# Kernel tuning notes

Hardware: AMD Instinct MI355X
Metric: run time of the kernel (lower is better)

## Reference

```python
import jax, jax.numpy as jnp
import numpy as np
from jax import lax

B, T = 16, 1000
IN_DIM = 257
CTX = 3            # left + 1 + right
FEAT = CTX * IN_DIM  # 771
H = 512
L = 2              # SRU layers
KN = 9             # conv kernels
KS = 6             # conv kernel size


def setup_inputs() -> dict:
    key = jax.random.key(0)
    ks = jax.random.split(key, 10)
    n = jax.random.normal
    return {
        "inputs": n(ks[0], (B, T, FEAT), jnp.float32),
        "W_in": n(ks[1], (FEAT, H), jnp.float32) / np.sqrt(FEAT),
        "b_in": jnp.zeros((H,), jnp.float32),
        "W_rnn": n(ks[2], (L, H, 3 * H), jnp.float32) / np.sqrt(H),
        "v_rnn": n(ks[3], (L, 2 * H), jnp.float32) * 0.1,
        "b_rnn": jnp.zeros((L, 2 * H), jnp.float32),
        "conv_k": n(ks[4], (KN, 1, KS, KS), jnp.float32) * 0.05,
        "conv_b": jnp.zeros((KN,), jnp.float32),
        "W_out": n(ks[5], (H * KN, FEAT), jnp.float32) / np.sqrt(H * KN),
        "b_out": jnp.zeros((FEAT,), jnp.float32),
    }


def _sru_layer(x, W, v, b):
    # x: (T, B, H) time-major; SRU: c_t = f_t*c_{t-1} + (1-f_t)*(W x_t),
    # highway h_t = r_t*c_t + (1-r_t)*x_t; gates peek at c_{t-1} via v.
    U = jnp.einsum("tbh,hk->tbk", x, W)          # (T, B, 3H)
    xt, fp, rp = jnp.split(U, 3, axis=-1)
    vf, vr = jnp.split(v, 2)
    bf, br = jnp.split(b, 2)

    def step(c, inp):
        xt_t, fp_t, rp_t, xin_t = inp
        f = jax.nn.sigmoid(fp_t + vf * c + bf)
        c_new = f * c + (1.0 - f) * xt_t
        r = jax.nn.sigmoid(rp_t + vr * c + br)
        h = r * c_new + (1.0 - r) * xin_t
        return c_new, h

    c0 = jnp.zeros(x.shape[1:], x.dtype)
    _, hs = lax.scan(step, c0, (xt, fp, rp, x))
    return hs


def reference(inputs, W_in, b_in, W_rnn, v_rnn, b_rnn, conv_k, conv_b, W_out, b_out):
    # input layer: Linear + Tanh
    h = jnp.tanh(jnp.einsum("btf,fh->bth", inputs, W_in) + b_in)  # (B,T,H)
    x = jnp.transpose(h, (1, 0, 2))                               # (T,B,H)
    for l in range(L):
        x = _sru_layer(x, W_rnn[l], v_rnn[l], b_rnn[l])
    h = jnp.transpose(x, (1, 0, 2))[:, None]                      # (B,1,T,H)

    # Conv2d with asymmetric pad (left/top 3, right/bottom 2), +bias, tanh
    y = lax.conv_general_dilated(
        h, conv_k, window_strides=(1, 1), padding=[(3, 2), (3, 2)],
        dimension_numbers=("NCHW", "OIHW", "NCHW"))
    y = jnp.tanh(y + conv_b[None, :, None, None])                 # (B,KN,T,H)
    # MaxPool2d(3, stride=1, padding=1)
    y = lax.reduce_window(y, -jnp.inf, lax.max, (1, 1, 3, 3), (1, 1, 1, 1),
                          [(0, 0), (0, 0), (1, 1), (1, 1)])

    # (B,KN,T,H) -> (B,T,H,KN) -> (B,T,H*KN)  (matches torch double transpose)
    y = jnp.transpose(y, (0, 2, 3, 1)).reshape(B, T, H * KN)
    mask = jax.nn.sigmoid(jnp.einsum("btf,fo->bto", y, W_out) + b_out)
    out = mask * inputs
    return out[:, :, IN_DIM:2 * IN_DIM]  # center frame (left_context slice)
```

## Files before the change

kernel.cpp:

```cpp
#include <hip/hip_runtime.h>
#include <hip/hip_bf16.h>

#define B_    16
#define T_    1000
#define FEAT  771
#define FEATP 800
#define H_    512
#define H3    1536
#define KN_   9
#define KHID  4608
#define M_    16000
#define NOUT  257
#define KSLICES 3

typedef _Float16 half8 __attribute__((ext_vector_type(8)));
typedef _Float16 half4 __attribute__((ext_vector_type(4)));
typedef _Float16 half2v __attribute__((ext_vector_type(2)));
typedef float    floatx4 __attribute__((ext_vector_type(4)));

__device__ inline float tanh_fast(float z) {
    return 1.0f - 2.0f / (1.0f + __expf(2.0f * z));
}
__device__ inline float sigmoid_fast(float z) {
    return 1.0f / (1.0f + __expf(-z));
}

__device__ inline void gload16(const _Float16* g, _Float16* l) {
    __builtin_amdgcn_global_load_lds(
        (const __attribute__((address_space(1))) void*)g,
        (__attribute__((address_space(3))) void*)l, 16, 0, 0);
}

__global__ void convert_inputs(const float* __restrict__ in, _Float16* __restrict__ A1) {
    size_t i = (size_t)blockIdx.x * 256 + threadIdx.x;
    if (i >= (size_t)M_ * FEATP) return;
    size_t r = i / FEATP;
    int   cc = (int)(i % FEATP);
    A1[i] = (cc < FEAT) ? (_Float16)in[r * FEAT + cc] : (_Float16)0.f;
}

__global__ __launch_bounds__(256) void transpose_w(
    const float* __restrict__ W, _Float16* __restrict__ Wt,
    int K, int N, int ldw, int coloff, int Kp, int perm9)
{
    __shared__ float tile[32][33];
    const int kb = blockIdx.x * 32;
    const int nb = blockIdx.y * 32;
    const int tx = threadIdx.x & 31;
    const int ty = threadIdx.x >> 5;
    #pragma unroll
    for (int r = ty; r < 32; r += 8) {
        const int k = kb + r, n = nb + tx;
        tile[r][tx] = (k < K && n < N) ? W[(size_t)k * ldw + coloff + n] : 0.f;
    }
    __syncthreads();
    #pragma unroll
    for (int r = ty; r < 32; r += 8) {
        const int n = nb + r, k = kb + tx;
        if (n < N && k < Kp) {
            size_t kidx = (size_t)k;
            if (perm9) kidx = (size_t)(k % 9) * 512 + (size_t)(k / 9);
            Wt[(size_t)n * Kp + kidx] = (_Float16)tile[tx][r];
        }
    }
}

template <int EPI>
__global__ __launch_bounds__(256) void gemm_kernel(
    const _Float16* __restrict__ A, const _Float16* __restrict__ Bt,
    int Kp, int nk, int Nb,
    _Float16* __restrict__ Ch, float* __restrict__ Cf, int ldc,
    const float* __restrict__ bias)
{
    __shared__ __align__(16) _Float16 As[128][32];
    __shared__ __align__(16) _Float16 Bs[128][32];

    const int tid  = threadIdx.x;
    const int m0   = blockIdx.x * 128;
    const int n0   = blockIdx.y * 128;
    const int koff = blockIdx.z * (nk << 5);
    const int wave = tid >> 6;
    const int lane = tid & 63;
    const int wr   = (wave >> 1) << 6;
    const int wc   = (wave & 1) << 6;
    const int lrow = lane & 15;
    const int lq   = lane >> 4;

    const int srow0  = wave * 32 + (lane >> 2);
    const int schunk = (lane & 3) * 8;
    const _Float16* aSrc = A  + (size_t)(m0 + srow0) * Kp + koff + schunk;
    const _Float16* bSrc = Bt + (size_t)(n0 + srow0) * Kp + koff + schunk;
    _Float16* aDst0 = &As[wave * 32][0];
    _Float16* aDst1 = &As[wave * 32 + 16][0];
    _Float16* bDst0 = &Bs[wave * 32][0];
    _Float16* bDst1 = &Bs[wave * 32 + 16][0];
    const size_t rstep = (size_t)16 * Kp;

    floatx4 acc[4][4];
    #pragma unroll
    for (int i = 0; i < 4; ++i)
        #pragma unroll
        for (int j = 0; j < 4; ++j)
            #pragma unroll
            for (int r = 0; r < 4; ++r) acc[i][j][r] = 0.f;

    for (int kc = 0; kc < nk; ++kc) {
        __syncthreads();
        gload16(aSrc,         aDst0);
        gload16(aSrc + rstep, aDst1);
        gload16(bSrc,         bDst0);
        gload16(bSrc + rstep, bDst1);
        aSrc += 32; bSrc += 32;
        __syncthreads();

        half8 af[4], bfr[4];
        #pragma unroll
        for (int i = 0; i < 4; ++i) af[i]  = *(const half8*)(&As[wr + i * 16 + lrow][lq * 8]);
        #pragma unroll
        for (int j = 0; j < 4; ++j) bfr[j] = *(const half8*)(&Bs[wc + j * 16 + lrow][lq * 8]);
        #pragma unroll
        for (int i = 0; i < 4; ++i)
            #pragma unroll
            for (int j = 0; j < 4; ++j)
                acc[i][j] = __builtin_amdgcn_mfma_f32_16x16x32_f16(af[i], bfr[j], acc[i][j], 0, 0, 0);
    }

    #pragma unroll
    for (int j = 0; j < 4; ++j) {
        const int col = n0 + wc + j * 16 + lrow;
        if (col >= Nb) continue;
        #pragma unroll
        for (int i = 0; i < 4; ++i) {
            #pragma unroll
            for (int r = 0; r < 4; ++r) {
                const int row = m0 + wr + i * 16 + lq * 4 + r;
                float v = acc[i][j][r];
                if constexpr (EPI == 0) {
                    float z = v + bias[col];
                    Ch[(size_t)row * ldc + col] = (_Float16)tanh_fast(z);
                } else if constexpr (EPI == 1) {
                    Ch[(size_t)(col >> 9) * ((size_t)M_ * 512) + (size_t)row * 512 + (col & 511)] = (_Float16)v;
                } else {
                    Cf[(size_t)blockIdx.z * M_ * NOUT + (size_t)row * NOUT + col] = v;
                }
            }
        }
    }
}

__global__ __launch_bounds__(256) void reduce_out(
    const float* __restrict__ Cp, const float* __restrict__ bias,
    const float* __restrict__ aux, float* __restrict__ out)
{
    const size_t i = (size_t)blockIdx.x * 256 + threadIdx.x;
    if (i >= (size_t)M_ * NOUT) return;
    const int row = (int)(i / NOUT);
    const int col = (int)(i % NOUT);
    float s = Cp[i] + Cp[i + (size_t)M_ * NOUT] + Cp[i + 2 * (size_t)M_ * NOUT];
    out[i] = sigmoid_fast(s + bias[col]) * aux[(size_t)row * FEAT + 257 + col];
}

__global__ __launch_bounds__(256) void repack_u(
    const _Float16* __restrict__ U,
    const _Float16* __restrict__ X,
    _Float16* __restrict__ Upk)
{
    const size_t i = (size_t)blockIdx.x * 256 + threadIdx.x;
    if (i >= (size_t)M_ * 128) return;
    const size_t base = i << 2;
    const half4 a = *(const half4*)(U + base);
    const half4 f = *(const half4*)(U + (size_t)M_ * 512 + base);
    const half4 r = *(const half4*)(U + 2 * (size_t)M_ * 512 + base);
    const half4 x = *(const half4*)(X + base);
    half8 lo, hi;
    lo[0] = a[0]; lo[1] = f[0]; lo[2] = r[0]; lo[3] = x[0];
    lo[4] = a[1]; lo[5] = f[1]; lo[6] = r[1]; lo[7] = x[1];
    hi[0] = a[2]; hi[1] = f[2]; hi[2] = r[2]; hi[3] = x[2];
    hi[4] = a[3]; hi[5] = f[3]; hi[6] = r[3]; hi[7] = x[3];
    *(half8*)(Upk + base * 4)     = lo;
    *(half8*)(Upk + base * 4 + 8) = hi;
}

__global__ __launch_bounds__(64) void sru_scan(
    const _Float16* __restrict__ Upk, _Float16* __restrict__ Xout,
    const float* __restrict__ v, const float* __restrict__ bg)
{
    const int gid = blockIdx.x * 64 + threadIdx.x;
    const int b = gid >> 9;
    const int h = gid & 511;
    const float vf = v[h],      vr = v[512 + h];
    const float bf = bg[h],     br = bg[512 + h];

    const _Float16* p = Upk + ((size_t)b * T_ * 512 + h) * 4;
    _Float16* ox = Xout + (size_t)b * T_ * 512 + h;

    half4 buf[20];
    #pragma unroll
    for (int j = 0; j < 20; ++j) buf[j] = *(const half4*)(p + (size_t)j * 2048);

    float c = 0.f;
    for (int t0 = 0; t0 < T_; t0 += 20) {
        #pragma unroll
        for (int j = 0; j < 20; ++j) {
            const int t = t0 + j;
            const half4 cur = buf[j];
            const int tn = t + 20;
            if (tn < T_) buf[j] = *(const half4*)(p + (size_t)tn * 2048);
            const float xt = (float)cur[0];
            const float fp = (float)cur[1];
            const float rp = (float)cur[2];
            const float x  = (float)cur[3];
            const float f  = sigmoid_fast(fp + vf * c + bf);
            const float r  = sigmoid_fast(rp + vr * c + br);
            const float cn = f * c + (1.0f - f) * xt;
            const float hO = r * cn + (1.0f - r) * x;
            ox[(size_t)t * 512] = (_Float16)hO;
            c = cn;
        }
    }
}

template <int JJ>
__device__ inline floatx4 window4(floatx4 a, floatx4 b, float r8) {
    floatx4 w;
    if constexpr (JJ == 0)      { w = a; }
    else if constexpr (JJ == 1) { w[0] = a[1]; w[1] = a[2]; w[2] = a[3]; w[3] = b[0]; }
    else if constexpr (JJ == 2) { w[0] = a[2]; w[1] = a[3]; w[2] = b[0]; w[3] = b[1]; }
    else if constexpr (JJ == 3) { w[0] = a[3]; w[1] = b[0]; w[2] = b[1]; w[3] = b[2]; }
    else if constexpr (JJ == 4) { w = b; }
    else                        { w[0] = b[1]; w[1] = b[2]; w[2] = b[3]; w[3] = r8; }
    return w;
}

#define CVW 76

__global__ __launch_bounds__(320) void conv_pool(
    const _Float16* __restrict__ X, const float* __restrict__ ck,
    const float* __restrict__ cb, _Float16* __restrict__ A3)
{
    __shared__ __align__(16) float    in_s[23][76];
    __shared__ __align__(16) _Float16 cv[9][18][CVW];
    const int tid = threadIdx.x;
    int bi = blockIdx.x;
    const int th = bi & 7;  bi >>= 3;
    const int tt = bi % 63;
    const int b  = bi / 63;
    const int t0 = tt * 16, h0 = th * 64;

    for (int i = tid; i < 23 * 76; i += 320) {
        const int r = i / 76, cc = i % 76;
        const int gt = t0 - 4 + r, gh = h0 - 4 + cc;
        float val = 0.f;
        if (gt >= 0 && gt < T_ && gh >= 0 && gh < H_)
            val = (float)X[((size_t)b * T_ + gt) * H_ + gh];
        in_s[r][cc] = val;
    }
    __syncthreads();

    if (tid < 306) {
        const int pt = tid / 17;
        const int co = (tid % 17) * 4;
        const float* inb = &in_s[pt][co];

        const int ct = t0 - 1 + pt;
        const bool rok = (ct >= 0) && (ct < T_);
        const int chb = h0 - 1 + co;
        const bool ok0 = rok && (chb + 0 >= 0) && (chb + 0 < H_);
        const bool ok1 = rok && (chb + 1 >= 0) && (chb + 1 < H_);
        const bool ok2 = rok && (chb + 2 >= 0) && (chb + 2 < H_);
        const bool ok3 = rok && (chb + 3 >= 0) && (chb + 3 < H_);

        #define EMIT_K(K, VV)                                                  \
        {                                                                      \
            const floatx4 vz = (VV);                                           \
            half4 o;                                                           \
            o[0] = ok0 ? (_Float16)vz[0] : (_Float16)(-65504.f);               \
            o[1] = ok1 ? (_Float16)vz[1] : (_Float16)(-65504.f);               \
            o[2] = ok2 ? (_Float16)vz[2] : (_Float16)(-65504.f);               \
            o[3] = ok3 ? (_Float16)vz[3] : (_Float16)(-65504.f);               \
            *(half4*)(&cv[K][pt][co]) = o;                                     \
        }

        {
            floatx4 c0 = 0.f, c1 = 0.f, c2 = 0.f, c3 = 0.f, c4 = 0.f;
            #pragma unroll 1
            for (int ii = 0; ii < 6; ++ii) {
                const float* row = inb + ii * 76;
                const floatx4 ra = *(const floatx4*)(row);
                const floatx4 rb = *(const floatx4*)(row + 4);
                const float   r8 = row[8];
                const float* wt = ck + ii * 6;
                #define TAP0(J)                                                \
                {                                                              \
                    const floatx4 win = window4<J>(ra, rb, r8);                \
                    c0 += wt[0 * 36 + (J)] * win;                              \
                    c1 += wt[1 * 36 + (J)] * win;                              \
                    c2 += wt[2 * 36 + (J)] * win;                              \
                    c3 += wt[3 * 36 + (J)] * win;                              \
                    c4 += wt[4 * 36 + (J)] * win;                              \
                }
                TAP0(0) TAP0(1) TAP0(2) TAP0(3) TAP0(4) TAP0(5)
                #undef TAP0
            }
            EMIT_K(0, c0) EMIT_K(1, c1) EMIT_K(2, c2) EMIT_K(3, c3) EMIT_K(4, c4)
        }
        {
            floatx4 c0 = 0.f, c1 = 0.f, c2 = 0.f, c3 = 0.f;
            #pragma unroll 1
            for (int ii = 0; ii < 6; ++ii) {
                const float* row = inb + ii * 76;
                const floatx4 ra = *(const floatx4*)(row);
                const floatx4 rb = *(const floatx4*)(row + 4);
                const float   r8 = row[8];
                const float* wt = ck + 5 * 36 + ii * 6;
                #define TAP1(J)                                                \
                {                                                              \
                    const floatx4 win = window4<J>(ra, rb, r8);                \
                    c0 += wt[0 * 36 + (J)] * win;                              \
                    c1 += wt[1 * 36 + (J)] * win;                              \
                    c2 += wt[2 * 36 + (J)] * win;                              \
                    c3 += wt[3 * 36 + (J)] * win;                              \
                }
                TAP1(0) TAP1(1) TAP1(2) TAP1(3) TAP1(4) TAP1(5)
                #undef TAP1
            }
            EMIT_K(5, c0) EMIT_K(6, c1) EMIT_K(7, c2) EMIT_K(8, c3)
        }
        #undef EMIT_K
    }
    __syncthreads();

    if (tid < 256) {
        const int pt = tid >> 4;
        const int gt = t0 + pt;
        if (gt < T_) {
            const int ph = (tid & 15) * 4;
            _Float16* dst = A3 + ((size_t)b * T_ + gt) * KHID + (h0 + ph);
            #pragma unroll
            for (int k = 0; k < 9; ++k) {
                float q0 = -1e30f, q1 = -1e30f, q2 = -1e30f, q3 = -1e30f;
                #pragma unroll
                for (int dr = 0; dr < 3; ++dr) {
                    const _Float16* cr = &cv[k][pt + dr][ph];
                    const half4  a = *(const half4*)(cr);
                    const half2v bq = *(const half2v*)(cr + 4);
                    const float v0 = (float)a[0], v1 = (float)a[1], v2 = (float)a[2];
                    const float v3 = (float)a[3], v4 = (float)bq[0], v5 = (float)bq[1];
                    const float t01 = fmaxf(v1, v2);
                    const float t34 = fmaxf(v3, v4);
                    q0 = fmaxf(q0, fmaxf(v0, t01));
                    q1 = fmaxf(q1, fmaxf(t01, v3));
                    q2 = fmaxf(q2, fmaxf(v2, t34));
                    q3 = fmaxf(q3, fmaxf(t34, v5));
                }
                const float bk = cb[k];
                half4 o;
                o[0] = (_Float16)tanh_fast(q0 + bk);
                o[1] = (_Float16)tanh_fast(q1 + bk);
                o[2] = (_Float16)tanh_fast(q2 + bk);
                o[3] = (_Float16)tanh_fast(q3 + bk);
                *(half4*)(dst + (size_t)k * 512) = o;
            }
        }
    }
}

extern "C" void kernel_launch(void* const* d_in, const int* in_sizes, int n_in,
                              void* d_out, int out_size, void* d_ws, size_t ws_size,
                              hipStream_t stream) {
    const float* inputs = (const float*)d_in[0];
    const float* W_in   = (const float*)d_in[1];
    const float* b_in   = (const float*)d_in[2];
    const float* W_rnn  = (const float*)d_in[3];
    const float* v_rnn  = (const float*)d_in[4];
    const float* b_rnn  = (const float*)d_in[5];
    const float* conv_k = (const float*)d_in[6];
    const float* conv_b = (const float*)d_in[7];
    const float* W_out  = (const float*)d_in[8];
    const float* b_out  = (const float*)d_in[9];
    float* out = (float*)d_out;

    char* ws = (char*)d_ws;
    size_t off = 0;
    auto take = [&](size_t bytes) -> char* {
        off = (off + 255) & ~(size_t)255;
        char* p = ws + off;
        off += bytes;
        return p;
    };
    _Float16* W3T  = (_Float16*)take((size_t)NOUT * KHID * 2);
    _Float16* A1   = (_Float16*)take((size_t)M_ * FEATP * 2);
    _Float16* W1T  = (_Float16*)take((size_t)H_ * FEATP * 2);
    _Float16* W2T0 = (_Float16*)take((size_t)H3 * H_ * 2);
    _Float16* W2T1 = (_Float16*)take((size_t)H3 * H_ * 2);
    _Float16* X0   = (_Float16*)take((size_t)M_ * H_ * 2);
    _Float16* X1   = (_Float16*)take((size_t)M_ * H_ * 2);
    _Float16* U    = (_Float16*)take(3 * (size_t)M_ * 512 * 2);
    _Float16* A3   = (_Float16*)take((size_t)M_ * KHID * 2);
    _Float16* Upk = A3;
    float* Cp = (float*)A1;
    _Float16* X2 = X0;

    {
        size_t n = (size_t)M_ * FEATP;
        convert_inputs<<<dim3((unsigned)((n + 255) / 256)), 256, 0, stream>>>(inputs, A1);
    }
    transpose_w<<<dim3(25, 16), 256, 0, stream>>>(W_in, W1T, FEAT, H_, H_, 0, FEATP, 0);
    transpose_w<<<dim3(16, 48), 256, 0, stream>>>(W_rnn, W2T0, H_, H3, H3, 0, H_, 0);
    transpose_w<<<dim3(16, 48), 256, 0, stream>>>(W_rnn + (size_t)H_ * H3, W2T1, H_, H3, H3, 0, H_, 0);
    transpose_w<<<dim3(144, 9), 256, 0, stream>>>(W_out, W3T, KHID, NOUT, FEAT, 257, KHID, 1);

    const unsigned nrep = (unsigned)(((size_t)M_ * 128 + 255) / 256);

    gemm_kernel<0><<<dim3(125, 4), 256, 0, stream>>>(A1, W1T, FEATP, 25, H_, X0, nullptr, H_, b_in);

    gemm_kernel<1><<<dim3(125, 12), 256, 0, stream>>>(X0, W2T0, H_, 16, H3, U, nullptr, 0, nullptr);
    repack_u<<<dim3(nrep), 256, 0, stream>>>(U, X0, Upk);
    sru_scan<<<dim3(128), 64, 0, stream>>>(Upk, X1, v_rnn, b_rnn);

    gemm_kernel<1><<<dim3(125, 12), 256, 0, stream>>>(X1, W2T1, H_, 16, H3, U, nullptr, 0, nullptr);
    repack_u<<<dim3(nrep), 256, 0, stream>>>(U, X1, Upk);
    sru_scan<<<dim3(128), 64, 0, stream>>>(Upk, X2, v_rnn + 1024, b_rnn + 1024);

    conv_pool<<<dim3(16 * 63 * 8), 320, 0, stream>>>(X2, conv_k, conv_b, A3);

    gemm_kernel<3><<<dim3(125, 3, KSLICES), 256, 0, stream>>>(A3, W3T, KHID, 144 / KSLICES, NOUT, nullptr, Cp, 0, nullptr);
    {
        const unsigned nred = (unsigned)(((size_t)M_ * NOUT + 255) / 256);
        reduce_out<<<dim3(nred), 256, 0, stream>>>(Cp, b_out + 257, inputs, out);
    }
}
```

Measured before the change: 820.0 us.

## Use packed fp16 FMA in conv and drop SRU repack kernel

The conv stage now keeps its input tile in fp16 shared memory and accumulates all nine filters with packed half2 FMAs, using weights pre-packed as duplicated fp16 pairs by a new tiny kernel. This roughly halves the conv ALU work but accumulates 36 taps in fp16, which costs accuracy. Separately, the repack_u kernel is removed and sru_scan reads the four planar U/X streams directly as scalar 16-bit loads. That saves a full pass over U, but the scan now issues four narrow loads per step instead of one 8-byte load.

```diff
diff --git a/kernel.cpp b/kernel.cpp
--- a/kernel.cpp
+++ b/kernel.cpp
@@ -16,6 +16,7 @@
 typedef _Float16 half8 __attribute__((ext_vector_type(8)));
 typedef _Float16 half4 __attribute__((ext_vector_type(4)));
 typedef _Float16 half2v __attribute__((ext_vector_type(2)));
+typedef _Float16 h2 __attribute__((ext_vector_type(2)));
 typedef float    floatx4 __attribute__((ext_vector_type(4)));
 
 __device__ inline float tanh_fast(float z) {
@@ -29,6 +30,16 @@
     __builtin_amdgcn_global_load_lds(
         (const __attribute__((address_space(1))) void*)g,
         (__attribute__((address_space(3))) void*)l, 16, 0, 0);
+}
+
+__device__ inline h2 pkfma(unsigned int w, unsigned int x, h2 c) {
+    const h2 a = __builtin_bit_cast(h2, w);
+    const h2 b = __builtin_bit_cast(h2, x);
+#if __has_builtin(__builtin_elementwise_fma)
+    return __builtin_elementwise_fma(a, b, c);
+#else
+    return a * b + c;
+#endif
 }
 
 __global__ void convert_inputs(const float* __restrict__ in, _Float16* __restrict__ A1) {
@@ -37,6 +48,15 @@
     size_t r = i / FEATP;
     int   cc = (int)(i % FEATP);
     A1[i] = (cc < FEAT) ? (_Float16)in[r * FEAT + cc] : (_Float16)0.f;
+}
+
+__global__ void pack_ck(const float* __restrict__ ck, unsigned int* __restrict__ ckp) {
+    const int i = threadIdx.x;
+    if (i < 9 * 36) {
+        const _Float16 w = (_Float16)ck[i];
+        const unsigned short u = __builtin_bit_cast(unsigned short, w);
+        ckp[i] = ((unsigned int)u << 16) | u;
+    }
 }
 
 __global__ __launch_bounds__(256) void transpose_w(
@@ -160,29 +180,10 @@
     out[i] = sigmoid_fast(s + bias[col]) * aux[(size_t)row * FEAT + 257 + col];
 }
 
-__global__ __launch_bounds__(256) void repack_u(
+__global__ __launch_bounds__(64) void sru_scan(
     const _Float16* __restrict__ U,
     const _Float16* __restrict__ X,
-    _Float16* __restrict__ Upk)
-{
-    const size_t i = (size_t)blockIdx.x * 256 + threadIdx.x;
-    if (i >= (size_t)M_ * 128) return;
-    const size_t base = i << 2;
-    const half4 a = *(const half4*)(U + base);
-    const half4 f = *(const half4*)(U + (size_t)M_ * 512 + base);
-    const half4 r = *(const half4*)(U + 2 * (size_t)M_ * 512 + base);
-    const half4 x = *(const half4*)(X + base);
-    half8 lo, hi;
-    lo[0] = a[0]; lo[1] = f[0]; lo[2] = r[0]; lo[3] = x[0];
-    lo[4] = a[1]; lo[5] = f[1]; lo[6] = r[1]; lo[7] = x[1];
-    hi[0] = a[2]; hi[1] = f[2]; hi[2] = r[2]; hi[3] = x[2];
-    hi[4] = a[3]; hi[5] = f[3]; hi[6] = r[3]; hi[7] = x[3];
-    *(half8*)(Upk + base * 4)     = lo;
-    *(half8*)(Upk + base * 4 + 8) = hi;
-}
-
-__global__ __launch_bounds__(64) void sru_scan(
-    const _Float16* __restrict__ Upk, _Float16* __restrict__ Xout,
+    _Float16* __restrict__ Xout,
     const float* __restrict__ v, const float* __restrict__ bg)
 {
     const int gid = blockIdx.x * 64 + threadIdx.x;
@@ -191,25 +192,37 @@
     const float vf = v[h],      vr = v[512 + h];
     const float bf = bg[h],     br = bg[512 + h];
 
-    const _Float16* p = Upk + ((size_t)b * T_ * 512 + h) * 4;
+    const unsigned short* pa = (const unsigned short*)U + (size_t)b * T_ * 512 + h;
+    const unsigned short* pf = pa + (size_t)M_ * 512;
+    const unsigned short* pr = pa + 2 * (size_t)M_ * 512;
+    const unsigned short* px = (const unsigned short*)X + (size_t)b * T_ * 512 + h;
     _Float16* ox = Xout + (size_t)b * T_ * 512 + h;
 
-    half4 buf[20];
+    unsigned short ba[20], bb[20], bc[20], bd[20];
     #pragma unroll
-    for (int j = 0; j < 20; ++j) buf[j] = *(const half4*)(p + (size_t)j * 2048);
+    for (int j = 0; j < 20; ++j) {
+        ba[j] = pa[(size_t)j * 512];
+        bb[j] = pf[(size_t)j * 512];
+        bc[j] = pr[(size_t)j * 512];
+        bd[j] = px[(size_t)j * 512];
+    }
 
     float c = 0.f;
     for (int t0 = 0; t0 < T_; t0 += 20) {
         #pragma unroll
         for (int j = 0; j < 20; ++j) {
             const int t = t0 + j;
-            const half4 cur = buf[j];
+            const float xt = (float)__builtin_bit_cast(_Float16, ba[j]);
+            const float fp = (float)__builtin_bit_cast(_Float16, bb[j]);
+            const float rp = (float)__builtin_bit_cast(_Float16, bc[j]);
+            const float x  = (float)__builtin_bit_cast(_Float16, bd[j]);
             const int tn = t + 20;
-            if (tn < T_) buf[j] = *(const half4*)(p + (size_t)tn * 2048);
-            const float xt = (float)cur[0];
-            const float fp = (float)cur[1];
-            const float rp = (float)cur[2];
-            const float x  = (float)cur[3];
+            if (tn < T_) {
+                ba[j] = pa[(size_t)tn * 512];
+                bb[j] = pf[(size_t)tn * 512];
+                bc[j] = pr[(size_t)tn * 512];
+                bd[j] = px[(size_t)tn * 512];
+            }
             const float f  = sigmoid_fast(fp + vf * c + bf);
             const float r  = sigmoid_fast(rp + vr * c + br);
             const float cn = f * c + (1.0f - f) * xt;
@@ -220,25 +233,13 @@
     }
 }
 
-template <int JJ>
-__device__ inline floatx4 window4(floatx4 a, floatx4 b, float r8) {
-    floatx4 w;
-    if constexpr (JJ == 0)      { w = a; }
-    else if constexpr (JJ == 1) { w[0] = a[1]; w[1] = a[2]; w[2] = a[3]; w[3] = b[0]; }
-    else if constexpr (JJ == 2) { w[0] = a[2]; w[1] = a[3]; w[2] = b[0]; w[3] = b[1]; }
-    else if constexpr (JJ == 3) { w[0] = a[3]; w[1] = b[0]; w[2] = b[1]; w[3] = b[2]; }
-    else if constexpr (JJ == 4) { w = b; }
-    else                        { w[0] = b[1]; w[1] = b[2]; w[2] = b[3]; w[3] = r8; }
-    return w;
-}
-
 #define CVW 76
 
 __global__ __launch_bounds__(320) void conv_pool(
-    const _Float16* __restrict__ X, const float* __restrict__ ck,
+    const _Float16* __restrict__ X, const unsigned int* __restrict__ ckp,
     const float* __restrict__ cb, _Float16* __restrict__ A3)
 {
-    __shared__ __align__(16) float    in_s[23][76];
+    __shared__ __align__(16) _Float16 in_s[23][80];
     __shared__ __align__(16) _Float16 cv[9][18][CVW];
     const int tid = threadIdx.x;
     int bi = blockIdx.x;
@@ -250,9 +251,9 @@
     for (int i = tid; i < 23 * 76; i += 320) {
         const int r = i / 76, cc = i % 76;
         const int gt = t0 - 4 + r, gh = h0 - 4 + cc;
-        float val = 0.f;
+        _Float16 val = (_Float16)0.f;
         if (gt >= 0 && gt < T_ && gh >= 0 && gh < H_)
-            val = (float)X[((size_t)b * T_ + gt) * H_ + gh];
+            val = X[((size_t)b * T_ + gt) * H_ + gh];
         in_s[r][cc] = val;
     }
     __syncthreads();
@@ -260,7 +261,6 @@
     if (tid < 306) {
         const int pt = tid / 17;
         const int co = (tid % 17) * 4;
-        const float* inb = &in_s[pt][co];
 
         const int ct = t0 - 1 + pt;
         const bool rok = (ct >= 0) && (ct < T_);
@@ -270,63 +270,48 @@
         const bool ok2 = rok && (chb + 2 >= 0) && (chb + 2 < H_);
         const bool ok3 = rok && (chb + 3 >= 0) && (chb + 3 < H_);
 
-        #define EMIT_K(K, VV)                                                  \
-        {                                                                      \
-            const floatx4 vz = (VV);                                           \
-            half4 o;                                                           \
-            o[0] = ok0 ? (_Float16)vz[0] : (_Float16)(-65504.f);               \
-            o[1] = ok1 ? (_Float16)vz[1] : (_Float16)(-65504.f);               \
-            o[2] = ok2 ? (_Float16)vz[2] : (_Float16)(-65504.f);               \
-            o[3] = ok3 ? (_Float16)vz[3] : (_Float16)(-65504.f);               \
-            *(half4*)(&cv[K][pt][co]) = o;                                     \
-        }
-
-        {
-            floatx4 c0 = 0.f, c1 = 0.f, c2 = 0.f, c3 = 0.f, c4 = 0.f;
-            #pragma unroll 1
-            for (int ii = 0; ii < 6; ++ii) {
-                const float* row = inb + ii * 76;
-                const floatx4 ra = *(const floatx4*)(row);
-                const floatx4 rb = *(const floatx4*)(row + 4);
-                const float   r8 = row[8];
-                const float* wt = ck + ii * 6;
-                #define TAP0(J)                                                \
-                {                                                              \
-                    const floatx4 win = window4<J>(ra, rb, r8);                \
-                    c0 += wt[0 * 36 + (J)] * win;                              \
-                    c1 += wt[1 * 36 + (J)] * win;                              \
-                    c2 += wt[2 * 36 + (J)] * win;                              \
-                    c3 += wt[3 * 36 + (J)] * win;                              \
-                    c4 += wt[4 * 36 + (J)] * win;                              \
-                }
-                TAP0(0) TAP0(1) TAP0(2) TAP0(3) TAP0(4) TAP0(5)
-                #undef TAP0
+        h2 acc0[9], acc1[9];
+        #pragma unroll
+        for (int k = 0; k < 9; ++k) {
+            acc0[k][0] = (_Float16)0.f; acc0[k][1] = (_Float16)0.f;
+            acc1[k][0] = (_Float16)0.f; acc1[k][1] = (_Float16)0.f;
+        }
+
+        #pragma unroll 1
+        for (int ii = 0; ii < 6; ++ii) {
+            const unsigned int* rw = (const unsigned int*)&in_s[pt + ii][co];
+            const uint2 a01 = *(const uint2*)(rw);
+            const uint2 a23 = *(const uint2*)(rw + 2);
+            const unsigned int A0 = a01.x, A1v = a01.y, A2 = a23.x, A3v = a23.y;
+            const unsigned int A4 = rw[4];
+            const unsigned int M0 = (A0  >> 16) | (A1v << 16);
+            const unsigned int M1 = (A1v >> 16) | (A2  << 16);
+            const unsigned int M2 = (A2  >> 16) | (A3v << 16);
+            const unsigned int M3 = (A3v >> 16) | (A4  << 16);
+
+            const unsigned int* wt = ckp + ii * 6;
+            #pragma unroll
+            for (int k = 0; k < 9; ++k) {
+                const unsigned int* wk = wt + k * 36;
+                acc0[k] = pkfma(wk[0], A0,  acc0[k]);  acc1[k] = pkfma(wk[0], A1v, acc1[k]);
+                acc0[k] = pkfma(wk[1], M0,  acc0[k]);  acc1[k] = pkfma(wk[1], M1,  acc1[k]);
+                acc0[k] = pkfma(wk[2], A1v, acc0[k]);  acc1[k] = pkfma(wk[2], A2,  acc1[k]);
+                acc0[k] = pkfma(wk[3], M1,  acc0[k]);  acc1[k] = pkfma(wk[3], M2,  acc1[k]);
+                acc0[k] = pkfma(wk[4], A2,  acc0[k]);  acc1[k] = pkfma(wk[4], A3v, acc1[k]);
+                acc0[k] = pkfma(wk[5], M2,  acc0[k]);  acc1[k] = pkfma(wk[5], M3,  acc1[k]);
             }
-            EMIT_K(0, c0) EMIT_K(1, c1) EMIT_K(2, c2) EMIT_K(3, c3) EMIT_K(4, c4)
-        }
-        {
-            floatx4 c0 = 0.f, c1 = 0.f, c2 = 0.f, c3 = 0.f;
-            #pragma unroll 1
-            for (int ii = 0; ii < 6; ++ii) {
-                const float* row = inb + ii * 76;
-                const floatx4 ra = *(const floatx4*)(row);
-                const floatx4 rb = *(const floatx4*)(row + 4);
-                const float   r8 = row[8];
-                const float* wt = ck + 5 * 36 + ii * 6;
-                #define TAP1(J)                                                \
-                {                                                              \
-                    const floatx4 win = window4<J>(ra, rb, r8);                \
-                    c0 += wt[0 * 36 + (J)] * win;                              \
-                    c1 += wt[1 * 36 + (J)] * win;                              \
-                    c2 += wt[2 * 36 + (J)] * win;                              \
-                    c3 += wt[3 * 36 + (J)] * win;                              \
-                }
-                TAP1(0) TAP1(1) TAP1(2) TAP1(3) TAP1(4) TAP1(5)
-                #undef TAP1
-            }
-            EMIT_K(5, c0) EMIT_K(6, c1) EMIT_K(7, c2) EMIT_K(8, c3)
-        }
-        #undef EMIT_K
+        }
+
+        const _Float16 NEG = (_Float16)(-65504.f);
+        #pragma unroll
+        for (int k = 0; k < 9; ++k) {
+            half4 o;
+            o[0] = ok0 ? acc0[k][0] : NEG;
+            o[1] = ok1 ? acc0[k][1] : NEG;
+            o[2] = ok2 ? acc1[k][0] : NEG;
+            o[3] = ok3 ? acc1[k][1] : NEG;
+            *(half4*)(&cv[k][pt][co]) = o;
+        }
     }
     __syncthreads();
 
@@ -397,7 +382,7 @@
     _Float16* X1   = (_Float16*)take((size_t)M_ * H_ * 2);
     _Float16* U    = (_Float16*)take(3 * (size_t)M_ * 512 * 2);
     _Float16* A3   = (_Float16*)take((size_t)M_ * KHID * 2);
-    _Float16* Upk = A3;
+    unsigned int* ckp = (unsigned int*)take(9 * 36 * 4);
     float* Cp = (float*)A1;
     _Float16* X2 = X0;
 
@@ -405,24 +390,21 @@
         size_t n = (size_t)M_ * FEATP;
         convert_inputs<<<dim3((unsigned)((n + 255) / 256)), 256, 0, stream>>>(inputs, A1);
     }
+    pack_ck<<<dim3(1), 384, 0, stream>>>(conv_k, ckp);
     transpose_w<<<dim3(25, 16), 256, 0, stream>>>(W_in, W1T, FEAT, H_, H_, 0, FEATP, 0);
     transpose_w<<<dim3(16, 48), 256, 0, stream>>>(W_rnn, W2T0, H_, H3, H3, 0, H_, 0);
     transpose_w<<<dim3(16, 48), 256, 0, stream>>>(W_rnn + (size_t)H_ * H3, W2T1, H_, H3, H3, 0, H_, 0);
     transpose_w<<<dim3(144, 9), 256, 0, stream>>>(W_out, W3T, KHID, NOUT, FEAT, 257, KHID, 1);
 
-    const unsigned nrep = (unsigned)(((size_t)M_ * 128 + 255) / 256);
-
     gemm_kernel<0><<<dim3(125, 4), 256, 0, stream>>>(A1, W1T, FEATP, 25, H_, X0, nullptr, H_, b_in);
 
     gemm_kernel<1><<<dim3(125, 12), 256, 0, stream>>>(X0, W2T0, H_, 16, H3, U, nullptr, 0, nullptr);
-    repack_u<<<dim3(nrep), 256, 0, stream>>>(U, X0, Upk);
-    sru_scan<<<dim3(128), 64, 0, stream>>>(Upk, X1, v_rnn, b_rnn);
+    sru_scan<<<dim3(128), 64, 0, stream>>>(U, X0, X1, v_rnn, b_rnn);
 
     gemm_kernel<1><<<dim3(125, 12), 256, 0, stream>>>(X1, W2T1, H_, 16, H3, U, nullptr, 0, nullptr);
-    repack_u<<<dim3(nrep), 256, 0, stream>>>(U, X1, Upk);
-    sru_scan<<<dim3(128), 64, 0, stream>>>(Upk, X2, v_rnn + 1024, b_rnn + 1024);
-
-    conv_pool<<<dim3(16 * 63 * 8), 320, 0, stream>>>(X2, conv_k, conv_b, A3);
+    sru_scan<<<dim3(128), 64, 0, stream>>>(U, X1, X2, v_rnn + 1024, b_rnn + 1024);
+
+    conv_pool<<<dim3(16 * 63 * 8), 320, 0, stream>>>(X2, ckp, conv_b, A3);
 
     gemm_kernel<3><<<dim3(125, 3, KSLICES), 256, 0, stream>>>(A3, W3T, KHID, 144 / KSLICES, NOUT, nullptr, Cp, 0, nullptr);
     {
```

New measurement: 1.485 ms. 1.81x slower.
